# Optimization experiments

Measured on AMD Instinct MI355X. Metric: run time of the kernel, lower is better.

The kernel has to match this reference:

```python
import jax, jax.numpy as jnp
import numpy as np

N_HEADS = 16

def setup_inputs() -> dict:
    key = jax.random.key(0)
    k1, k2, k3, k4, k5 = jax.random.split(key, 5)
    B, S, D = 2, 2048, 1024
    x = jax.random.normal(k1, (B, S, D), dtype=jnp.float32)
    # parameters scaled ~ fan-in to keep softmax logits sane
    w_in = jax.random.normal(k2, (D, 3 * D), dtype=jnp.float32) * (1.0 / np.sqrt(D))
    b_in = jax.random.normal(k3, (3 * D,), dtype=jnp.float32) * 0.02
    w_out = jax.random.normal(k4, (D, D), dtype=jnp.float32) * (1.0 / np.sqrt(D))
    b_out = jax.random.normal(k5, (D,), dtype=jnp.float32) * 0.02
    return {"x": x, "w_in": w_in, "b_in": b_in, "w_out": w_out, "b_out": b_out,
            "causal_mask": 1}


def reference(x, w_in, b_in, w_out, b_out, causal_mask):
    B, S, D = x.shape
    H = N_HEADS
    dh = D // H
    qkv = x @ w_in + b_in                        # [B, S, 3D]
    q, k, v = jnp.split(qkv, 3, axis=-1)          # each [B, S, D]
    q = q.reshape(B, S, H, dh)
    k = k.reshape(B, S, H, dh)
    v = v.reshape(B, S, H, dh)
    # scores: [B, H, Sq, Sk]
    scores = jnp.einsum("bqhd,bkhd->bhqk", q, k)
    if causal_mask:
        mask = jnp.triu(jnp.ones((S, S), dtype=bool), k=1)
        scores = jnp.where(mask, -jnp.inf, scores)
    scores = scores / jnp.sqrt(jnp.asarray(dh, dtype=scores.dtype))
    weight = jax.nn.softmax(scores, axis=-1)
    out = jnp.einsum("bhqk,bkhd->bqhd", weight, v).reshape(B, S, D)
    return out @ w_out + b_out
```

## Files before the change

### kernel.cpp

```cpp
#include <hip/hip_runtime.h>
#include <hip/hip_bf16.h>

typedef __attribute__((ext_vector_type(8))) short short8;
typedef __attribute__((ext_vector_type(4))) short s16x4;
typedef __attribute__((ext_vector_type(4))) float f32x4;
typedef unsigned short u16;

__device__ inline u16 f2bf(float f) {
    union { float f; unsigned u; } x{f};
    unsigned r = (x.u + 0x7fff + ((x.u >> 16) & 1)) >> 16;
    return (u16)r;
}

__device__ inline void glds16(const u16* g, u16* l) {
    __builtin_amdgcn_global_load_lds(
        (const __attribute__((address_space(1))) void*)g,
        (__attribute__((address_space(3))) void*)l, 16, 0, 0);
}

__global__ __launch_bounds__(256) void cvt_bf16(const float* __restrict__ in,
                                                u16* __restrict__ out, int n) {
    int i = (blockIdx.x * 256 + threadIdx.x) * 4;
    if (i >= n) return;
    float4 v = *(const float4*)&in[i];
    uint2 o;
    o.x = (unsigned)f2bf(v.x) | ((unsigned)f2bf(v.y) << 16);
    o.y = (unsigned)f2bf(v.z) | ((unsigned)f2bf(v.w) << 16);
    *(uint2*)&out[i] = o;
}

__global__ __launch_bounds__(256) void transpose_cvt(const float* __restrict__ W,
                                                     u16* __restrict__ Wt,
                                                     int K, int N) {
    __shared__ float tile[32][33];
    int n0 = blockIdx.x * 32, k0 = blockIdx.y * 32;
    int tx = threadIdx.x, ty = threadIdx.y;
    for (int i = 0; i < 32; i += 8)
        tile[ty + i][tx] = W[(size_t)(k0 + ty + i) * N + n0 + tx];
    __syncthreads();
    for (int i = 0; i < 32; i += 8)
        Wt[(size_t)(n0 + ty + i) * K + k0 + tx] = f2bf(tile[tx][ty + i]);
}

__global__ __launch_bounds__(256) void transpose_v(const u16* __restrict__ qkv,
                                                   u16* __restrict__ VT) {
    __shared__ u16 t[32][33];
    int s0 = blockIdx.x * 32, d0 = blockIdx.y * 32, bh = blockIdx.z;
    int b = bh >> 4, h = bh & 15;
    int tx = threadIdx.x, ty = threadIdx.y;
    const u16* Vp = qkv + (size_t)(b * 2048) * 3072 + 2048 + h * 64;
    for (int i = 0; i < 32; i += 8)
        t[ty + i][tx] = Vp[(size_t)(s0 + ty + i) * 3072 + d0 + tx];
    __syncthreads();
    u16* Vr = VT + (size_t)bh * 64 * 2048;
    for (int i = 0; i < 32; i += 8)
        Vr[(size_t)(d0 + ty + i) * 2048 + s0 + tx] = t[tx][ty + i];
}

#define BM 128
#define BN 128
#define BK 64
__global__ __launch_bounds__(256) void gemm_bt(const u16* __restrict__ A,
                                               const u16* __restrict__ Bt,
                                               const float* __restrict__ bias,
                                               void* __restrict__ C,
                                               int M, int N, int K, int c_is_f32) {
    __shared__ u16 smem[2 * BM * BK + 2048];
    u16* As = smem;
    u16* Bs = smem + BM * BK;

    int tid = threadIdx.x;
    int wave = tid >> 6, lane = tid & 63;
    int quad = lane >> 4, l16 = lane & 15;
    int wm = (wave >> 1) * 64, wn = (wave & 1) * 64;

    int nm = M / BM, nn = N / BN;
    const int GM = 8;
    int per_group = GM * nn;
    int group = blockIdx.x / per_group;
    int rem = blockIdx.x % per_group;
    int first_m = group * GM;
    int gsz = (nm - first_m < GM) ? (nm - first_m) : GM;
    int m0 = (first_m + rem % gsz) * BM;
    int n0 = (rem / gsz) * BN;

    f32x4 acc[4][4] = {};

    for (int k0 = 0; k0 < K; k0 += BK) {
        __syncthreads();
        for (int i = 0; i < 4; i++) {
            int c = tid + i * 256;
            int r = c >> 3, cc = c & 7;
            int gsrc = (cc ^ (r & 7)) * 8;
            glds16(&A[(size_t)(m0 + r) * K + k0 + gsrc], As + c * 8);
            glds16(&Bt[(size_t)(n0 + r) * K + k0 + gsrc], Bs + c * 8);
        }
        __syncthreads();
        for (int ks = 0; ks < 2; ks++) {
            short8 af[4], bf[4];
            for (int i = 0; i < 4; i++) {
                int row = wm + i * 16 + l16;
                int slot = (ks * 4 + quad) ^ (row & 7);
                af[i] = *(short8*)&As[row * BK + slot * 8];
            }
            for (int j = 0; j < 4; j++) {
                int row = wn + j * 16 + l16;
                int slot = (ks * 4 + quad) ^ (row & 7);
                bf[j] = *(short8*)&Bs[row * BK + slot * 8];
            }
            for (int i = 0; i < 4; i++)
                for (int j = 0; j < 4; j++)
                    acc[i][j] = __builtin_amdgcn_mfma_f32_16x16x32_bf16(
                        af[i], bf[j], acc[i][j], 0, 0, 0);
        }
    }

    if (c_is_f32) {
        for (int i = 0; i < 4; i++)
            for (int j = 0; j < 4; j++) {
                int col = n0 + wn + j * 16 + l16;
                float bv = bias ? bias[col] : 0.f;
                for (int r = 0; r < 4; r++) {
                    int row = m0 + wm + i * 16 + quad * 4 + r;
                    ((float*)C)[(size_t)row * N + col] = acc[i][j][r] + bv;
                }
            }
    } else {
        __syncthreads();
        u16 (*buf)[136] = (u16(*)[136])smem;
        for (int i = 0; i < 4; i++)
            for (int j = 0; j < 4; j++) {
                int col = wn + j * 16 + l16;
                float bv = bias ? bias[n0 + col] : 0.f;
                for (int r = 0; r < 4; r++)
                    buf[wm + i * 16 + quad * 4 + r][col] = f2bf(acc[i][j][r] + bv);
            }
        __syncthreads();
        u16* Cb = (u16*)C;
        for (int it = 0; it < 8; it++) {
            int c = tid + it * 256;
            int row = c >> 4, k8 = c & 15;
            uint4 v = *(uint4*)&buf[row][k8 * 8];
            *(uint4*)&Cb[(size_t)(m0 + row) * N + n0 + k8 * 8] = v;
        }
    }
}

__global__ __launch_bounds__(256) void attn_kernel(const u16* __restrict__ qkv,
                                                   const u16* __restrict__ VT,
                                                   u16* __restrict__ out) {
    const int S = 2048, D = 1024, stride = 3072;
    int idx = blockIdx.x;
    int qt = 15 - (idx >> 5);
    int bh = idx & 31;
    int b = bh >> 4, h = bh & 15;
    int tid = threadIdx.x;
    int wave = tid >> 6, lane = tid & 63;
    int quad = lane >> 4, l16 = lane & 15;

    __shared__ u16 Klds[2][64 * 64];
    __shared__ u16 Vlds[2][64 * 64];
    __shared__ u16 Obuf[4][32][72];

    const u16* Qp = qkv + (size_t)(b * S) * stride + h * 64;
    const u16* Kp = Qp + D;
    const u16* Vtp = VT + (size_t)bh * 64 * S;

    short8 qf[2][2];
    for (int f = 0; f < 2; f++) {
        int qrow = qt * 128 + wave * 32 + f * 16 + l16;
        qf[f][0] = *(const short8*)&Qp[(size_t)qrow * stride + quad * 8];
        qf[f][1] = *(const short8*)&Qp[(size_t)qrow * stride + 32 + quad * 8];
    }

    f32x4 O[2][4] = {};
    float lsum[2] = {};

    int ntiles = 2 * qt + 2;
    const float sc = 0.125f * 1.44269504f;

    auto stage = [&](int kt, int bsel) {
        for (int i = 0; i < 2; i++) {
            int c = tid + i * 256;
            int r = c >> 3, cc = c & 7;
            int gsrc = (cc ^ (r & 7)) * 8;
            glds16(&Kp[(size_t)(kt * 64 + r) * stride + gsrc], &Klds[bsel][c * 8]);
            glds16(&Vtp[(size_t)r * S + kt * 64 + gsrc], &Vlds[bsel][c * 8]);
        }
    };

    stage(0, 0);

    for (int kt = 0; kt < ntiles; kt++) {
        int cur = kt & 1;
        __syncthreads();
        if (kt + 1 < ntiles) stage(kt + 1, cur ^ 1);

        short8 kf[4][2];
        for (int nb = 0; nb < 4; nb++) {
            int r = nb * 16 + l16;
            kf[nb][0] = *(short8*)&Klds[cur][r * 64 + ((0 + quad) ^ (r & 7)) * 8];
            kf[nb][1] = *(short8*)&Klds[cur][r * 64 + ((4 + quad) ^ (r & 7)) * 8];
        }
        f32x4 st[2][4];
        for (int f = 0; f < 2; f++)
            for (int nb = 0; nb < 4; nb++) {
                f32x4 t = {};
                t = __builtin_amdgcn_mfma_f32_16x16x32_bf16(kf[nb][0], qf[f][0], t, 0, 0, 0);
                t = __builtin_amdgcn_mfma_f32_16x16x32_bf16(kf[nb][1], qf[f][1], t, 0, 0, 0);
                st[f][nb] = t;
            }

        if (kt >= 2 * qt) {
            for (int f = 0; f < 2; f++) {
                int qabs = qt * 128 + wave * 32 + f * 16 + l16;
                for (int nb = 0; nb < 4; nb++) {
                    int kb = kt * 64 + nb * 16 + quad * 4;
                    for (int r = 0; r < 4; r++) {
                        float e = __builtin_amdgcn_exp2f(st[f][nb][r] * sc);
                        st[f][nb][r] = (kb + r <= qabs) ? e : 0.f;
                    }
                }
            }
        } else {
            for (int f = 0; f < 2; f++)
                for (int nb = 0; nb < 4; nb++)
                    for (int r = 0; r < 4; r++)
                        st[f][nb][r] = __builtin_amdgcn_exp2f(st[f][nb][r] * sc);
        }

        s16x4 pf[2][4];
        for (int f = 0; f < 2; f++)
            for (int nb = 0; nb < 4; nb++) {
                lsum[f] += (st[f][nb][0] + st[f][nb][1]) +
                           (st[f][nb][2] + st[f][nb][3]);
                uint2 pk;
                pk.x = (unsigned)f2bf(st[f][nb][0]) | ((unsigned)f2bf(st[f][nb][1]) << 16);
                pk.y = (unsigned)f2bf(st[f][nb][2]) | ((unsigned)f2bf(st[f][nb][3]) << 16);
                pf[f][nb] = __builtin_bit_cast(s16x4, pk);
            }

        for (int db = 0; db < 4; db++) {
            int rr = db * 16 + l16;
            s16x4 vf[4];
            for (int kc = 0; kc < 4; kc++) {
                int g = kc * 2 + (quad >> 1);
                int slot = g ^ (rr & 7);
                vf[kc] = *(s16x4*)&Vlds[cur][rr * 64 + slot * 8 + (quad & 1) * 4];
            }
            for (int f = 0; f < 2; f++)
                for (int kc = 0; kc < 4; kc++)
                    O[f][db] = __builtin_amdgcn_mfma_f32_16x16x16bf16_1k(
                        pf[f][kc], vf[kc], O[f][db], 0, 0, 0);
        }
    }

    float rinv[2][4];
    for (int f = 0; f < 2; f++) {
        float v = lsum[f];
        v += __shfl_xor(v, 16);
        v += __shfl_xor(v, 32);
        for (int r = 0; r < 4; r++)
            rinv[f][r] = 1.f / __shfl(v, (lane & 48) | (quad * 4 + r));
    }
    for (int f = 0; f < 2; f++)
        for (int db = 0; db < 4; db++)
            for (int r = 0; r < 4; r++)
                Obuf[wave][f * 16 + quad * 4 + r][db * 16 + l16] =
                    f2bf(O[f][db][r] * rinv[f][r]);
    __asm__ volatile("s_waitcnt lgkmcnt(0)" ::: "memory");
    for (int i = 0; i < 4; i++) {
        int c = i * 64 + lane;
        int row = c >> 3, cc = c & 7;
        uint4 v = *(uint4*)&Obuf[wave][row][cc * 8];
        int grow = qt * 128 + wave * 32 + row;
        *(uint4*)&out[(size_t)(b * S + grow) * D + h * 64 + cc * 8] = v;
    }
}

extern "C" void kernel_launch(void* const* d_in, const int* in_sizes, int n_in,
                              void* d_out, int out_size, void* d_ws, size_t ws_size,
                              hipStream_t stream) {
    const float* x     = (const float*)d_in[0];
    const float* w_in  = (const float*)d_in[1];
    const float* b_in  = (const float*)d_in[2];
    const float* w_out = (const float*)d_in[3];
    const float* b_out = (const float*)d_in[4];

    const int Bsz = 2, S = 2048, D = 1024, H = 16;
    const int M = Bsz * S;
    const int N1 = 3 * D;

    u16* ws    = (u16*)d_ws;
    u16* Xb    = ws;
    u16* WtIn  = Xb + (size_t)M * D;
    u16* WtOut = WtIn + (size_t)N1 * D;
    u16* qkvb  = WtOut + (size_t)D * D;
    u16* attnb = qkvb + (size_t)M * N1;
    u16* Vt    = Xb;

    cvt_bf16<<<(M * D) / 1024, 256, 0, stream>>>(x, Xb, M * D);
    transpose_cvt<<<dim3(N1 / 32, D / 32), dim3(32, 8), 0, stream>>>(w_in, WtIn, D, N1);
    transpose_cvt<<<dim3(D / 32, D / 32), dim3(32, 8), 0, stream>>>(w_out, WtOut, D, D);
    gemm_bt<<<(M / BM) * (N1 / BN), 256, 0, stream>>>(Xb, WtIn, b_in, qkvb,
                                                      M, N1, D, 0);
    transpose_v<<<dim3(S / 32, 2, Bsz * H), dim3(32, 8), 0, stream>>>(qkvb, Vt);
    attn_kernel<<<16 * Bsz * H, 256, 0, stream>>>(qkvb, Vt, attnb);
    gemm_bt<<<(M / BM) * (D / BN), 256, 0, stream>>>(attnb, WtOut, b_out, d_out,
                                                     M, D, D, 1);
}
```

Baseline: 204.5 us.

## Pair causal query tiles per block, fold softmax scale into Q, fuse prep kernels

The attention kernel now runs 256 blocks of 512 threads. Each block handles two query tiles (p and 15-p) one after the other, so every block does an equal amount of causal work, and each wave owns 16 query rows instead of 32. The softmax scale (times log2 e) is applied to Q in the QKV GEMM epilogue, which removes a multiply per score. A perm-based bf16 pack replaces the scalar round-and-shift. The three preprocessing kernels are merged into one launch to cut launch overhead. The pack changes rounding slightly (round-half-up instead of round-to-even), and applying the scale before bf16 rounding of Q changes numerics a little.

```diff
diff --git a/kernel.cpp b/kernel.cpp
--- a/kernel.cpp
+++ b/kernel.cpp
@@ -12,29 +12,46 @@
     return (u16)r;
 }
 
+__device__ inline unsigned pkbf(float hi, float lo) {
+    unsigned a = __builtin_bit_cast(unsigned, hi) + 0x8000u;
+    unsigned b = __builtin_bit_cast(unsigned, lo) + 0x8000u;
+    return __builtin_amdgcn_perm(a, b, 0x07060302u);
+}
+
 __device__ inline void glds16(const u16* g, u16* l) {
     __builtin_amdgcn_global_load_lds(
         (const __attribute__((address_space(1))) void*)g,
         (__attribute__((address_space(3))) void*)l, 16, 0, 0);
 }
 
-__global__ __launch_bounds__(256) void cvt_bf16(const float* __restrict__ in,
-                                                u16* __restrict__ out, int n) {
-    int i = (blockIdx.x * 256 + threadIdx.x) * 4;
-    if (i >= n) return;
-    float4 v = *(const float4*)&in[i];
-    uint2 o;
-    o.x = (unsigned)f2bf(v.x) | ((unsigned)f2bf(v.y) << 16);
-    o.y = (unsigned)f2bf(v.z) | ((unsigned)f2bf(v.w) << 16);
-    *(uint2*)&out[i] = o;
-}
-
-__global__ __launch_bounds__(256) void transpose_cvt(const float* __restrict__ W,
-                                                     u16* __restrict__ Wt,
-                                                     int K, int N) {
+__global__ __launch_bounds__(256) void prep(const float* __restrict__ x,
+                                            const float* __restrict__ w_in,
+                                            const float* __restrict__ w_out,
+                                            u16* __restrict__ Xb,
+                                            u16* __restrict__ WtIn,
+                                            u16* __restrict__ WtOut) {
     __shared__ float tile[32][33];
-    int n0 = blockIdx.x * 32, k0 = blockIdx.y * 32;
-    int tx = threadIdx.x, ty = threadIdx.y;
+    int bx = blockIdx.x, tid = threadIdx.x;
+    if (bx < 4096) {
+        int i = (bx * 256 + tid) * 4;
+        float4 v = *(const float4*)&x[i];
+        uint2 o;
+        o.x = (unsigned)f2bf(v.x) | ((unsigned)f2bf(v.y) << 16);
+        o.y = (unsigned)f2bf(v.z) | ((unsigned)f2bf(v.w) << 16);
+        *(uint2*)&Xb[i] = o;
+        return;
+    }
+    const float* W; u16* Wt; int K, N, n0, k0;
+    if (bx < 7168) {
+        int b2 = bx - 4096;
+        W = w_in; Wt = WtIn; K = 1024; N = 3072;
+        n0 = (b2 % 96) * 32; k0 = (b2 / 96) * 32;
+    } else {
+        int b3 = bx - 7168;
+        W = w_out; Wt = WtOut; K = 1024; N = 1024;
+        n0 = (b3 & 31) * 32; k0 = (b3 >> 5) * 32;
+    }
+    int tx = tid & 31, ty = tid >> 5;
     for (int i = 0; i < 32; i += 8)
         tile[ty + i][tx] = W[(size_t)(k0 + ty + i) * N + n0 + tx];
     __syncthreads();
@@ -64,7 +81,8 @@
                                                const u16* __restrict__ Bt,
                                                const float* __restrict__ bias,
                                                void* __restrict__ C,
-                                               int M, int N, int K, int c_is_f32) {
+                                               int M, int N, int K, int c_is_f32,
+                                               int qcols, float qscale) {
     __shared__ u16 smem[2 * BM * BK + 2048];
     u16* As = smem;
     u16* Bs = smem + BM * BK;
@@ -132,8 +150,10 @@
             for (int j = 0; j < 4; j++) {
                 int col = wn + j * 16 + l16;
                 float bv = bias ? bias[n0 + col] : 0.f;
+                float scl = (n0 + col < qcols) ? qscale : 1.f;
                 for (int r = 0; r < 4; r++)
-                    buf[wm + i * 16 + quad * 4 + r][col] = f2bf(acc[i][j][r] + bv);
+                    buf[wm + i * 16 + quad * 4 + r][col] =
+                        f2bf((acc[i][j][r] + bv) * scl);
             }
         __syncthreads();
         u16* Cb = (u16*)C;
@@ -146,13 +166,13 @@
     }
 }
 
-__global__ __launch_bounds__(256) void attn_kernel(const u16* __restrict__ qkv,
+__global__ __launch_bounds__(512) void attn_kernel(const u16* __restrict__ qkv,
                                                    const u16* __restrict__ VT,
                                                    u16* __restrict__ out) {
     const int S = 2048, D = 1024, stride = 3072;
     int idx = blockIdx.x;
-    int qt = 15 - (idx >> 5);
-    int bh = idx & 31;
+    int p = idx >> 5, bh = idx & 31;
+    int qtb[2] = {15 - p, p};
     int b = bh >> 4, h = bh & 15;
     int tid = threadIdx.x;
     int wave = tid >> 6, lane = tid & 63;
@@ -160,41 +180,46 @@
 
     __shared__ u16 Klds[2][64 * 64];
     __shared__ u16 Vlds[2][64 * 64];
-    __shared__ u16 Obuf[4][32][72];
+    __shared__ u16 Obuf[8][16][72];
 
     const u16* Qp = qkv + (size_t)(b * S) * stride + h * 64;
     const u16* Kp = Qp + D;
     const u16* Vtp = VT + (size_t)bh * 64 * S;
 
     short8 qf[2][2];
-    for (int f = 0; f < 2; f++) {
-        int qrow = qt * 128 + wave * 32 + f * 16 + l16;
-        qf[f][0] = *(const short8*)&Qp[(size_t)qrow * stride + quad * 8];
-        qf[f][1] = *(const short8*)&Qp[(size_t)qrow * stride + 32 + quad * 8];
-    }
-
-    f32x4 O[2][4] = {};
-    float lsum[2] = {};
-
-    int ntiles = 2 * qt + 2;
-    const float sc = 0.125f * 1.44269504f;
+    for (int ph = 0; ph < 2; ph++) {
+        int qrow = qtb[ph] * 128 + wave * 16 + l16;
+        qf[ph][0] = *(const short8*)&Qp[(size_t)qrow * stride + quad * 8];
+        qf[ph][1] = *(const short8*)&Qp[(size_t)qrow * stride + 32 + quad * 8];
+    }
+
+    int nt0 = 2 * qtb[0] + 2;
+    int total = nt0 + 2 * qtb[1] + 2;
 
     auto stage = [&](int kt, int bsel) {
-        for (int i = 0; i < 2; i++) {
-            int c = tid + i * 256;
-            int r = c >> 3, cc = c & 7;
-            int gsrc = (cc ^ (r & 7)) * 8;
-            glds16(&Kp[(size_t)(kt * 64 + r) * stride + gsrc], &Klds[bsel][c * 8]);
-            glds16(&Vtp[(size_t)r * S + kt * 64 + gsrc], &Vlds[bsel][c * 8]);
-        }
+        int c = tid;
+        int r = c >> 3, cc = c & 7;
+        int gsrc = (cc ^ (r & 7)) * 8;
+        glds16(&Kp[(size_t)(kt * 64 + r) * stride + gsrc], &Klds[bsel][c * 8]);
+        glds16(&Vtp[(size_t)r * S + kt * 64 + gsrc], &Vlds[bsel][c * 8]);
     };
 
     stage(0, 0);
 
-    for (int kt = 0; kt < ntiles; kt++) {
-        int cur = kt & 1;
-        __syncthreads();
-        if (kt + 1 < ntiles) stage(kt + 1, cur ^ 1);
+    f32x4 O[4] = {};
+    float lsum = 0.f;
+
+    for (int it = 0; it < total; it++) {
+        int ph = (it >= nt0) ? 1 : 0;
+        int kt = ph ? it - nt0 : it;
+        int qt = qtb[ph];
+        int cur = it & 1;
+        __syncthreads();
+        if (it + 1 < total) {
+            int it2 = it + 1;
+            int k2 = (it2 >= nt0) ? it2 - nt0 : it2;
+            stage(k2, cur ^ 1);
+        }
 
         short8 kf[4][2];
         for (int nb = 0; nb < 4; nb++) {
@@ -202,79 +227,71 @@
             kf[nb][0] = *(short8*)&Klds[cur][r * 64 + ((0 + quad) ^ (r & 7)) * 8];
             kf[nb][1] = *(short8*)&Klds[cur][r * 64 + ((4 + quad) ^ (r & 7)) * 8];
         }
-        f32x4 st[2][4];
-        for (int f = 0; f < 2; f++)
+        f32x4 st[4];
+        for (int nb = 0; nb < 4; nb++) {
+            f32x4 t = {};
+            t = __builtin_amdgcn_mfma_f32_16x16x32_bf16(kf[nb][0], qf[ph][0], t, 0, 0, 0);
+            t = __builtin_amdgcn_mfma_f32_16x16x32_bf16(kf[nb][1], qf[ph][1], t, 0, 0, 0);
+            st[nb] = t;
+        }
+
+        if (kt >= 2 * qt) {
+            int qabs = qt * 128 + wave * 16 + l16;
             for (int nb = 0; nb < 4; nb++) {
-                f32x4 t = {};
-                t = __builtin_amdgcn_mfma_f32_16x16x32_bf16(kf[nb][0], qf[f][0], t, 0, 0, 0);
-                t = __builtin_amdgcn_mfma_f32_16x16x32_bf16(kf[nb][1], qf[f][1], t, 0, 0, 0);
-                st[f][nb] = t;
-            }
-
-        if (kt >= 2 * qt) {
-            for (int f = 0; f < 2; f++) {
-                int qabs = qt * 128 + wave * 32 + f * 16 + l16;
-                for (int nb = 0; nb < 4; nb++) {
-                    int kb = kt * 64 + nb * 16 + quad * 4;
-                    for (int r = 0; r < 4; r++) {
-                        float e = __builtin_amdgcn_exp2f(st[f][nb][r] * sc);
-                        st[f][nb][r] = (kb + r <= qabs) ? e : 0.f;
-                    }
+                int kb = kt * 64 + nb * 16 + quad * 4;
+                for (int r = 0; r < 4; r++) {
+                    float e = __builtin_amdgcn_exp2f(st[nb][r]);
+                    st[nb][r] = (kb + r <= qabs) ? e : 0.f;
                 }
             }
         } else {
-            for (int f = 0; f < 2; f++)
-                for (int nb = 0; nb < 4; nb++)
-                    for (int r = 0; r < 4; r++)
-                        st[f][nb][r] = __builtin_amdgcn_exp2f(st[f][nb][r] * sc);
-        }
-
-        s16x4 pf[2][4];
-        for (int f = 0; f < 2; f++)
-            for (int nb = 0; nb < 4; nb++) {
-                lsum[f] += (st[f][nb][0] + st[f][nb][1]) +
-                           (st[f][nb][2] + st[f][nb][3]);
-                uint2 pk;
-                pk.x = (unsigned)f2bf(st[f][nb][0]) | ((unsigned)f2bf(st[f][nb][1]) << 16);
-                pk.y = (unsigned)f2bf(st[f][nb][2]) | ((unsigned)f2bf(st[f][nb][3]) << 16);
-                pf[f][nb] = __builtin_bit_cast(s16x4, pk);
-            }
+            for (int nb = 0; nb < 4; nb++)
+                for (int r = 0; r < 4; r++)
+                    st[nb][r] = __builtin_amdgcn_exp2f(st[nb][r]);
+        }
+
+        s16x4 pf[4];
+        for (int nb = 0; nb < 4; nb++) {
+            lsum += (st[nb][0] + st[nb][1]) + (st[nb][2] + st[nb][3]);
+            uint2 pk;
+            pk.x = pkbf(st[nb][1], st[nb][0]);
+            pk.y = pkbf(st[nb][3], st[nb][2]);
+            pf[nb] = __builtin_bit_cast(s16x4, pk);
+        }
 
         for (int db = 0; db < 4; db++) {
             int rr = db * 16 + l16;
-            s16x4 vf[4];
             for (int kc = 0; kc < 4; kc++) {
                 int g = kc * 2 + (quad >> 1);
                 int slot = g ^ (rr & 7);
-                vf[kc] = *(s16x4*)&Vlds[cur][rr * 64 + slot * 8 + (quad & 1) * 4];
-            }
-            for (int f = 0; f < 2; f++)
-                for (int kc = 0; kc < 4; kc++)
-                    O[f][db] = __builtin_amdgcn_mfma_f32_16x16x16bf16_1k(
-                        pf[f][kc], vf[kc], O[f][db], 0, 0, 0);
-        }
-    }
-
-    float rinv[2][4];
-    for (int f = 0; f < 2; f++) {
-        float v = lsum[f];
-        v += __shfl_xor(v, 16);
-        v += __shfl_xor(v, 32);
-        for (int r = 0; r < 4; r++)
-            rinv[f][r] = 1.f / __shfl(v, (lane & 48) | (quad * 4 + r));
-    }
-    for (int f = 0; f < 2; f++)
-        for (int db = 0; db < 4; db++)
+                s16x4 vf = *(s16x4*)&Vlds[cur][rr * 64 + slot * 8 + (quad & 1) * 4];
+                O[db] = __builtin_amdgcn_mfma_f32_16x16x16bf16_1k(
+                    pf[kc], vf, O[db], 0, 0, 0);
+            }
+        }
+
+        if (it == nt0 - 1 || it == total - 1) {
+            float v = lsum;
+            v += __shfl_xor(v, 16);
+            v += __shfl_xor(v, 32);
+            float rinv[4];
             for (int r = 0; r < 4; r++)
-                Obuf[wave][f * 16 + quad * 4 + r][db * 16 + l16] =
-                    f2bf(O[f][db][r] * rinv[f][r]);
-    __asm__ volatile("s_waitcnt lgkmcnt(0)" ::: "memory");
-    for (int i = 0; i < 4; i++) {
-        int c = i * 64 + lane;
-        int row = c >> 3, cc = c & 7;
-        uint4 v = *(uint4*)&Obuf[wave][row][cc * 8];
-        int grow = qt * 128 + wave * 32 + row;
-        *(uint4*)&out[(size_t)(b * S + grow) * D + h * 64 + cc * 8] = v;
+                rinv[r] = 1.f / __shfl(v, (lane & 48) | (quad * 4 + r));
+            for (int db = 0; db < 4; db++)
+                for (int r = 0; r < 4; r++)
+                    Obuf[wave][quad * 4 + r][db * 16 + l16] =
+                        f2bf(O[db][r] * rinv[r]);
+            __asm__ volatile("s_waitcnt lgkmcnt(0)" ::: "memory");
+            for (int i = 0; i < 2; i++) {
+                int c = i * 64 + lane;
+                int row = c >> 3, cc = c & 7;
+                uint4 vv = *(uint4*)&Obuf[wave][row][cc * 8];
+                int grow = qt * 128 + wave * 16 + row;
+                *(uint4*)&out[(size_t)(b * S + grow) * D + h * 64 + cc * 8] = vv;
+            }
+            for (int db = 0; db < 4; db++) O[db] = (f32x4){0.f, 0.f, 0.f, 0.f};
+            lsum = 0.f;
+        }
     }
 }
 
@@ -290,6 +307,7 @@
     const int Bsz = 2, S = 2048, D = 1024, H = 16;
     const int M = Bsz * S;
     const int N1 = 3 * D;
+    const float sc = 0.125f * 1.44269504f;
 
     u16* ws    = (u16*)d_ws;
     u16* Xb    = ws;
@@ -299,13 +317,11 @@
     u16* attnb = qkvb + (size_t)M * N1;
     u16* Vt    = Xb;
 
-    cvt_bf16<<<(M * D) / 1024, 256, 0, stream>>>(x, Xb, M * D);
-    transpose_cvt<<<dim3(N1 / 32, D / 32), dim3(32, 8), 0, stream>>>(w_in, WtIn, D, N1);
-    transpose_cvt<<<dim3(D / 32, D / 32), dim3(32, 8), 0, stream>>>(w_out, WtOut, D, D);
+    prep<<<8192, 256, 0, stream>>>(x, w_in, w_out, Xb, WtIn, WtOut);
     gemm_bt<<<(M / BM) * (N1 / BN), 256, 0, stream>>>(Xb, WtIn, b_in, qkvb,
-                                                      M, N1, D, 0);
+                                                      M, N1, D, 0, D, sc);
     transpose_v<<<dim3(S / 32, 2, Bsz * H), dim3(32, 8), 0, stream>>>(qkvb, Vt);
-    attn_kernel<<<16 * Bsz * H, 256, 0, stream>>>(qkvb, Vt, attnb);
+    attn_kernel<<<256, 512, 0, stream>>>(qkvb, Vt, attnb);
     gemm_bt<<<(M / BM) * (D / BN), 256, 0, stream>>>(attnb, WtOut, b_out, d_out,
-                                                     M, D, D, 1);
-}
+                                                     M, D, D, 1, 0, 1.f);
+}
```

New measurement: 192.1 us. -6.0%, faster.
